# Optimization experiments

Hardware: AMD Instinct MI355X
Metric: run time of the kernel (lower is better)

Reference implementation:

```python
import jax, jax.numpy as jnp
import numpy as np
from functools import partial

T_DEC, T_ENC = 64, 256
B, E, D = 32, 256, 512   # batch, audio_encoder_size(=input_size), decoder_hidden_size
N_MEL = 80               # spectral_size == n_mel_channels


def setup_inputs() -> dict:
    key = jax.random.key(0)
    ks = jax.random.split(key, 9)
    s = 0.02
    return {
        "decoder_inputs": jax.random.normal(ks[0], (T_DEC, B, E), jnp.float32),
        "alignment_inputs": jax.random.normal(ks[1], (T_ENC, B, E), jnp.float32),
        "W_att": jax.random.normal(ks[2], (E, D), jnp.float32) * s,      # LinearNorm(D->E, no bias)
        "W_ih": jax.random.normal(ks[3], (3 * D, 2 * E), jnp.float32) * s,  # GRUCell input weights (r,z,n)
        "W_hh": jax.random.normal(ks[4], (3 * D, D), jnp.float32) * s,      # GRUCell hidden weights
        "W_mel": jax.random.normal(ks[5], (N_MEL, D + E), jnp.float32) * s,
        "b_mel": jax.random.normal(ks[6], (N_MEL,), jnp.float32) * s,
        "W_gate": jax.random.normal(ks[7], (1, D + E), jnp.float32) * s,
        "b_gate": jax.random.normal(ks[8], (1,), jnp.float32) * s,
    }


def _decode_loop(decoder_inputs, alignment_inputs, W_att, W_ih, W_hh, W_mel, b_mel, W_gate, b_gate):
    Bd, Dd = decoder_inputs.shape[1], W_hh.shape[1]

    def step(h, dec_in):
        # --- Attention: per-feature softmax over encoder time, collapsed over features ---
        proj = h @ W_att.T                                  # (B, E)
        scores = alignment_inputs * proj[None]              # (T_enc, B, E)
        w = jax.nn.softmax(scores, axis=0)                  # softmax over encoder time
        tw = w.sum(axis=-1)                                 # (T_enc, B): sum of per-feature weights
        ctx = jnp.einsum('tb,tbe->be', tw, alignment_inputs)  # (B, E)
        # --- GRUCell (bias=False) ---
        x = jnp.concatenate([dec_in, ctx], axis=-1)         # (B, 2E)
        gi = x @ W_ih.T                                     # (B, 3D)
        gh = h @ W_hh.T                                     # (B, 3D)
        ir, iz, inn = jnp.split(gi, 3, axis=-1)
        hr, hz, hn = jnp.split(gh, 3, axis=-1)
        r = jax.nn.sigmoid(ir + hr)
        z = jax.nn.sigmoid(iz + hz)
        n = jnp.tanh(inn + r * hn)
        h_new = (1.0 - z) * n + z * h
        h_new = jax.nn.relu(h_new)                          # relu(dropout(h)), dropout=0
        # --- Output heads ---
        dhac = jnp.concatenate([ctx, h_new], axis=-1)       # (B, E+D)
        mel = dhac @ W_mel.T + b_mel                        # (B, N_MEL)
        gate = dhac @ W_gate.T + b_gate                     # (B, 1)
        return h_new, (mel, gate)

    # prepend zero init frame, drop last frame (teacher forcing, T_dec steps)
    init_frame = jnp.zeros((1,) + decoder_inputs.shape[1:], decoder_inputs.dtype)
    seq = jnp.concatenate([init_frame, decoder_inputs[:-1]], axis=0)
    h0 = jnp.zeros((Bd, Dd), decoder_inputs.dtype)
    _, (mels, gates) = jax.lax.scan(step, h0, seq)
    # parse_decoder_outputs
    n_mel = W_mel.shape[0]
    mel_out = mels.transpose(1, 0, 2).reshape(Bd, -1, n_mel).transpose(0, 2, 1)  # (B, n_mel, T_dec)
    gate_out = gates.transpose(1, 0, 2)                                          # (B, T_dec, 1)
    return mel_out, gate_out


def reference(decoder_inputs, alignment_inputs, W_att, W_ih, W_hh, W_mel, b_mel, W_gate, b_gate):
    return _decode_loop(decoder_inputs, alignment_inputs, W_att, W_ih, W_hh,
                        W_mel, b_mel, W_gate, b_gate)
```

## Files before the change

### kernel.cpp

```cpp
#include <hip/hip_runtime.h>
#include <hip/hip_bf16.h>


#define LOG2E 1.4426950408889634f
#define FLAGS_MAGIC 0x13572468u
#define SMEM_BYTES 150016
#define NBLK 98

typedef __attribute__((ext_vector_type(8))) short bf8;
typedef __attribute__((ext_vector_type(4))) float f32x4;
typedef __attribute__((ext_vector_type(4))) unsigned u32x4;
typedef unsigned long long ull;

#define EX2(x) exp2f(x)
#define MFMA16(a, b, c) __builtin_amdgcn_mfma_f32_16x16x32_bf16(a, b, c, 0, 0, 0)

struct Params {
  const float* dec;
  const float* ali;
  const float* watt;
  const float* wih;
  const float* whh;
  const float* wmel;
  const float* bmel;
  const float* wgate;
  const float* bgate;
  float* out;
  unsigned* bar;
  __hip_bfloat16* wihb;
  __hip_bfloat16* whhb;
  __hip_bfloat16* wmelgb;
  __hip_bfloat16* seqb;
  __hip_bfloat16* hbf;
  __hip_bfloat16* ctxb;
  unsigned* wattp;
};

__device__ __forceinline__ bf8 ldfrag(const __hip_bfloat16* p) { return *(const bf8*)p; }
__device__ __forceinline__ float sigm(float x) { return 1.0f / (1.0f + EX2(-x * LOG2E)); }
__device__ __forceinline__ float tanhfast(float x) {
  x = fminf(fmaxf(x, -15.0f), 15.0f);
  float e = EX2(x * (2.0f * LOG2E));
  return (e - 1.0f) / (e + 1.0f);
}
__device__ __forceinline__ float btof(unsigned v) { return __uint_as_float(v << 16); }
__device__ __forceinline__ unsigned short f2bfbits(float x) {
  __hip_bfloat16 h = __float2bfloat16(x);
  return *(unsigned short*)&h;
}
__device__ __forceinline__ unsigned sysld32(const unsigned* p) {
  return __hip_atomic_load(p, __ATOMIC_RELAXED, __HIP_MEMORY_SCOPE_SYSTEM);
}
__device__ __forceinline__ ull sysld64(const ull* p) {
  return __hip_atomic_load(p, __ATOMIC_RELAXED, __HIP_MEMORY_SCOPE_SYSTEM);
}
__device__ __forceinline__ void sysst32(unsigned* p, unsigned v) {
  __hip_atomic_store(p, v, __ATOMIC_RELAXED, __HIP_MEMORY_SCOPE_SYSTEM);
}
__device__ __forceinline__ void sysst64(ull* p, ull v) {
  __hip_atomic_store(p, v, __ATOMIC_RELAXED, __HIP_MEMORY_SCOPE_SYSTEM);
}
__device__ __forceinline__ void sysld16x4(u32x4* d0, u32x4* d1, u32x4* d2, u32x4* d3,
                                          const void* p0, const void* p1,
                                          const void* p2, const void* p3) {
  u32x4 a, b, c, d;
  asm volatile(
      "global_load_dwordx4 %0, %4, off sc0 sc1\n\t"
      "global_load_dwordx4 %1, %5, off sc0 sc1\n\t"
      "global_load_dwordx4 %2, %6, off sc0 sc1\n\t"
      "global_load_dwordx4 %3, %7, off sc0 sc1\n\t"
      "s_waitcnt vmcnt(0)"
      : "=&v"(a), "=&v"(b), "=&v"(c), "=&v"(d)
      : "v"(p0), "v"(p1), "v"(p2), "v"(p3)
      : "memory");
  *d0 = a; *d1 = b; *d2 = c; *d3 = d;
}
__device__ __forceinline__ void waitge(unsigned* w, unsigned tgt) {
  while (sysld32(w) < tgt) __builtin_amdgcn_s_sleep(1);
}

__device__ __forceinline__ void p0bar(unsigned* bar) {
  __syncthreads();
  if (threadIdx.x == 0) {
    __builtin_amdgcn_fence(__ATOMIC_RELEASE, "agent");
    __hip_atomic_fetch_add(bar + 16, 1u, __ATOMIC_RELAXED, __HIP_MEMORY_SCOPE_SYSTEM);
    while (sysld32(bar + 16) < (unsigned)NBLK) __builtin_amdgcn_s_sleep(1);
    __builtin_amdgcn_fence(__ATOMIC_ACQUIRE, "agent");
  }
  __syncthreads();
}

__device__ __forceinline__ void p0a_worker(const Params& p, int wid) {
  for (int i = wid; i < 2252800; i += 17408) {
    if (i < 786432) {
      p.wihb[i] = __float2bfloat16(p.wih[i]);
    } else if (i < 1572864) {
      int j = i - 786432;
      p.whhb[j] = __float2bfloat16(p.whh[j]);
    } else if (i < 2097152) {
      int j = i - 1572864;
      int s = j >> 13;
      p.seqb[j] = (s == 0) ? __float2bfloat16(0.0f) : __float2bfloat16(p.dec[j - 8192]);
    } else if (i < 2170880) {
      int j = i - 2097152;
      int r = j / 768, c = j - r * 768;
      float v = (r < 80) ? p.wmel[j] : ((r == 80) ? p.wgate[c] : 0.0f);
      p.wmelgb[j] = __float2bfloat16(v);
    } else if (i < 2236416) {
      int j = i - 2170880;
      int kp = j >> 8, e = j & 255;
      unsigned lo = f2bfbits(p.watt[e * 512 + 2 * kp]);
      unsigned hi = f2bfbits(p.watt[e * 512 + 2 * kp + 1]);
      p.wattp[j] = lo | (hi << 16);
    } else {
      int j = i - 2236416;
      p.hbf[j] = __float2bfloat16(0.0f);
    }
  }
}

__device__ __forceinline__ void stage_h_frag(__hip_bfloat16* hA,
                                             const __hip_bfloat16* hsrc, int tid) {
  const int lm = tid & 15, lq = (tid >> 4) & 3, wq = tid >> 6;
  const int dst_in = (lq * 16 + lm) * 8;
  const int i0 = wq, i1 = 8 + wq, i2 = 16 + wq, i3 = 24 + wq;
  auto soff = [&](int idx) {
    return ((idx >> 4) * 16 + lm) * 512 + (idx & 15) * 32 + lq * 8;
  };
  u32x4 a, b, c, d;
  sysld16x4(&a, &b, &c, &d, hsrc + soff(i0), hsrc + soff(i1), hsrc + soff(i2),
            hsrc + soff(i3));
  u32x4* dst = (u32x4*)hA;
  dst[(i0 * 512 + dst_in) >> 3] = a;
  dst[(i1 * 512 + dst_in) >> 3] = b;
  dst[(i2 * 512 + dst_in) >> 3] = c;
  dst[(i3 * 512 + dst_in) >> 3] = d;
}
__device__ __forceinline__ void stage_c2(__hip_bfloat16* cA,
                                         const __hip_bfloat16* csrc, int tid) {
  const int lm = tid & 15, lq = (tid >> 4) & 3, wq = tid >> 6;
  const int dst_in = (lq * 16 + lm) * 8;
  const int i0 = wq, i1 = 8 + wq, i2 = 16 + wq, i3 = 24 + wq;
  auto soff = [&](int idx) {
    int bb = (idx >> 4) * 16 + lm;
    int k = (idx & 15) * 32 + lq * 8;
    return ((k >> 8) * 32 + bb) * 256 + (k & 255);
  };
  u32x4 a, b, c, d;
  sysld16x4(&a, &b, &c, &d, csrc + soff(i0), csrc + soff(i1), csrc + soff(i2),
            csrc + soff(i3));
  u32x4* dst = (u32x4*)cA;
  dst[(i0 * 512 + dst_in) >> 3] = a;
  dst[(i1 * 512 + dst_in) >> 3] = b;
  dst[(i2 * 512 + dst_in) >> 3] = c;
  dst[(i3 * 512 + dst_in) >> 3] = d;
}

__global__ void __launch_bounds__(512, 1) rdec_kernel(Params p) {
  const int tid = threadIdx.x;
  const int bid = blockIdx.x;
  extern __shared__ char smem[];
  unsigned* hdone = p.bar + 32;
  unsigned* ctxdone = p.bar + 544;
  unsigned* meldone = p.bar + 1568;

  if (bid == 0) {
    for (int i = 1 + tid; i < 2624; i += 512) sysst32(p.bar + i, 0u);
    __syncthreads();
    if (tid == 0) sysst32(p.bar, FLAGS_MAGIC);
  }

  if (bid < 64) {
    const int b = bid >> 1, eh = bid & 1, hb = eh * 32 + b;
    unsigned short* alds = (unsigned short*)smem;
    float* fb = (float*)(smem + 133120);
    float* shh = fb;
    float* p2 = fb + 512;
    float* rz = fb + 640;
    float* red = fb + 768;
    float* twp = fb + 1280;
    float* tw = fb + 3328;
    float* cp = fb + 3584;
    unsigned short* pc16 = (unsigned short*)(fb + 4096);

    const int el = tid & 127, q = tid >> 7;
    const int eg = tid >> 6, tg = tid & 63;
    const int f = tid & 255, th = tid >> 8;

    for (int i = tid; i < 65536; i += 512) {
      int t = i >> 8, ee = i & 255;
      alds[ee * 260 + t] = f2bfbits(p.ali[t * 8192 + b * 256 + ee]);
    }
    if (tid == 0) {
      while (sysld32(p.bar) != FLAGS_MAGIC) __builtin_amdgcn_s_sleep(1);
    }
    p0bar(p.bar);
    unsigned wr[64];
#pragma unroll
    for (int i = 0; i < 64; ++i) wr[i] = p.wattp[(q * 64 + i) * 256 + eh * 128 + el];

    for (int s = 0; s < 64; ++s) {
      if (tid < 32) waitge(hdone + tid * 16, (unsigned)s);
      else if (tid < 34) waitge(meldone + (tid - 32) * 16, (s >= 4) ? (unsigned)(s - 3) : 0u);
      __syncthreads();
      if (tid < 128) {
        ull w = sysld64((const ull*)(p.hbf + (s & 3) * 16384 + b * 512) + tid);
        shh[tid * 4 + 0] = btof((unsigned)(w & 0xffff));
        shh[tid * 4 + 1] = btof((unsigned)((w >> 16) & 0xffff));
        shh[tid * 4 + 2] = btof((unsigned)((w >> 32) & 0xffff));
        shh[tid * 4 + 3] = btof((unsigned)((w >> 48) & 0xffff));
      }
      __syncthreads();
      {
        const float2* h2 = (const float2*)shh;
        float a0 = 0.f, a1 = 0.f;
#pragma unroll
        for (int i = 0; i < 64; i += 2) {
          unsigned w0 = wr[i], w1 = wr[i + 1];
          float2 h0 = h2[q * 64 + i], h1 = h2[q * 64 + i + 1];
          a0 = fmaf(__uint_as_float(w0 << 16), h0.x, a0);
          a0 = fmaf(__uint_as_float(w0 & 0xffff0000u), h0.y, a0);
          a1 = fmaf(__uint_as_float(w1 << 16), h1.x, a1);
          a1 = fmaf(__uint_as_float(w1 & 0xffff0000u), h1.y, a1);
        }
        red[q * 128 + el] = a0 + a1;
      }
      __syncthreads();
      if (tid < 128)
        p2[tid] = (red[tid] + red[128 + tid] + red[256 + tid] + red[384 + tid]) * LOG2E;
      __syncthreads();
      {
        const unsigned short* ap = alds + (eh * 128 + el) * 260 + q * 64;
        const float pp = p2[el];
        float z0 = 0.f, z1 = 0.f;
#pragma unroll 4
        for (int j = 0; j < 16; ++j) {
          ushort4 v = *(const ushort4*)(ap + j * 4);
          z0 += EX2(btof(v.x) * pp) + EX2(btof(v.y) * pp);
          z1 += EX2(btof(v.z) * pp) + EX2(btof(v.w) * pp);
        }
        red[q * 128 + el] = z0 + z1;
      }
      __syncthreads();
      if (tid < 128)
        rz[tid] = 1.0f / (red[tid] + red[128 + tid] + red[256 + tid] + red[384 + tid]);
      __syncthreads();
      {
        float t0 = 0.f, t1 = 0.f, t2 = 0.f, t3 = 0.f;
#pragma unroll 4
        for (int j = 0; j < 16; ++j) {
          const int e2 = eg * 16 + j;
          ushort4 v = *(const ushort4*)(alds + (eh * 128 + e2) * 260 + tg * 4);
          const float pp = p2[e2], rr = rz[e2];
          t0 = fmaf(EX2(btof(v.x) * pp), rr, t0);
          t1 = fmaf(EX2(btof(v.y) * pp), rr, t1);
          t2 = fmaf(EX2(btof(v.z) * pp), rr, t2);
          t3 = fmaf(EX2(btof(v.w) * pp), rr, t3);
        }
        *(float4*)(twp + eg * 256 + tg * 4) = make_float4(t0, t1, t2, t3);
      }
      __syncthreads();
      if (tid < 256) {
        float t0 = 0.f;
#pragma unroll
        for (int g = 0; g < 8; ++g) t0 += twp[g * 256 + tid];
        tw[tid] = t0;
      }
      __syncthreads();
      {
        const unsigned short* ap = alds + f * 260 + th * 128;
        const float4* twv = (const float4*)(tw + th * 128);
        float c0 = 0.f, c1 = 0.f;
#pragma unroll 4
        for (int j = 0; j < 32; ++j) {
          ushort4 v = *(const ushort4*)(ap + j * 4);
          float4 t4 = twv[j];
          c0 += t4.x * btof(v.x) + t4.y * btof(v.y);
          c1 += t4.z * btof(v.z) + t4.w * btof(v.w);
        }
        cp[th * 256 + f] = c0 + c1;
      }
      __syncthreads();
      if (tid < 256) pc16[tid] = f2bfbits(cp[tid] + cp[256 + tid]);
      __syncthreads();
      if (tid < 32) {
        ull* cs = (ull*)(p.ctxb + ((s & 3) * 64 + hb) * 256);
        const ull* ca = (const ull*)pc16;
        sysst64(cs + tid * 2, ca[tid * 2]);
        sysst64(cs + tid * 2 + 1, ca[tid * 2 + 1]);
      }
      __syncthreads();
      if (tid == 0) sysst32(ctxdone + hb * 16, (unsigned)(s + 1));
    }
  } else if (bid < 96) {
    const int dt = bid - 64;
    const int wv = tid >> 6;
    const bool act = wv < 6;
    const int l = tid & 63, lm = l & 15, lq = l >> 4;
    const int g = wv % 3, mt = wv / 3;
    const int am = mt * 16 + lm;
    const int brow = g * 512 + dt * 16 + lm;
    __hip_bfloat16* hA = (__hip_bfloat16*)smem;
    __hip_bfloat16* cA = (__hip_bfloat16*)(smem + 32768);
    float* pw = (float*)(smem + 65536);
    unsigned short* h16 = (unsigned short*)(smem + 74240);
    p0a_worker(p, (bid - 64) * 512 + tid);
    if (tid == 0) {
      while (sysld32(p.bar) != FLAGS_MAGIC) __builtin_amdgcn_s_sleep(1);
    }
    p0bar(p.bar);
    bf8 WH[16], WD[8], WC[8];
    if (act) {
#pragma unroll
      for (int kt = 0; kt < 16; ++kt) WH[kt] = ldfrag(p.whhb + brow * 512 + kt * 32 + lq * 8);
#pragma unroll
      for (int kt = 0; kt < 8; ++kt) WD[kt] = ldfrag(p.wihb + brow * 512 + kt * 32 + lq * 8);
#pragma unroll
      for (int kt = 0; kt < 8; ++kt) WC[kt] = ldfrag(p.wihb + brow * 512 + 256 + kt * 32 + lq * 8);
    }
    for (int s = 0; s < 64; ++s) {
      if (tid < 32) waitge(hdone + tid * 16, (unsigned)s);
      else if (tid < 34) waitge(meldone + (tid - 32) * 16, (s >= 4) ? (unsigned)(s - 3) : 0u);
      __syncthreads();
      stage_h_frag(hA, p.hbf + (s & 3) * 16384, tid);
      __syncthreads();
      f32x4 acc = {0.f, 0.f, 0.f, 0.f};
      f32x4 gi = {0.f, 0.f, 0.f, 0.f};
      if (act) {
#pragma unroll
        for (int kt = 0; kt < 16; ++kt) {
          bf8 a = ldfrag(hA + (mt * 16 + kt) * 512 + l * 8);
          acc = MFMA16(a, WH[kt], acc);
        }
        const __hip_bfloat16* seqp = p.seqb + s * 8192;
#pragma unroll
        for (int kt = 0; kt < 8; ++kt) {
          bf8 a = ldfrag(seqp + am * 256 + kt * 32 + lq * 8);
          gi = MFMA16(a, WD[kt], gi);
        }
      }
      if (tid < 64) waitge(ctxdone + tid * 16, (unsigned)(s + 1));
      __syncthreads();
      stage_c2(cA, p.ctxb + (s & 3) * 16384, tid);
      __syncthreads();
      if (act) {
#pragma unroll
        for (int kt = 0; kt < 16; ++kt) {
          bf8 a = ldfrag(cA + (mt * 16 + kt) * 512 + l * 8);
          gi = MFMA16(a, WC[kt & 7], gi);
        }
        if (g < 2) {
#pragma unroll
          for (int r = 0; r < 4; ++r) pw[(wv * 16 + lq * 4 + r) * 17 + lm] = acc[r] + gi[r];
        } else {
#pragma unroll
          for (int r = 0; r < 4; ++r) pw[(wv * 16 + lq * 4 + r) * 17 + lm] = acc[r];
#pragma unroll
          for (int r = 0; r < 4; ++r) pw[((6 + mt) * 16 + lq * 4 + r) * 17 + lm] = gi[r];
        }
      }
      __syncthreads();
      {
        const int bb = tid >> 4, dl = tid & 15;
        const int mtb = bb >> 4, bl = bb & 15;
        float rg = sigm(pw[((mtb * 3 + 0) * 16 + bl) * 17 + dl]);
        float zg = sigm(pw[((mtb * 3 + 1) * 16 + bl) * 17 + dl]);
        float hn = pw[((mtb * 3 + 2) * 16 + bl) * 17 + dl];
        float inn = pw[((6 + mtb) * 16 + bl) * 17 + dl];
        float nn = tanhfast(fmaf(rg, hn, inn));
        const int d = dt * 16 + dl;
        float ho = btof(((unsigned short*)hA)[((bb >> 4) * 16 + (d >> 5)) * 512 +
                                              (((d >> 3) & 3) * 16 + (bb & 15)) * 8 +
                                              (d & 7)]);
        float hnew = fmaxf(0.0f, fmaf(zg, ho - nn, nn));
        h16[bb * 16 + dl] = f2bfbits(hnew);
      }
      __syncthreads();
      if (tid < 256) {
        const int bb2 = tid >> 3, dp = tid & 7;
        unsigned v = (unsigned)h16[bb2 * 16 + dp * 2] |
                     ((unsigned)h16[bb2 * 16 + dp * 2 + 1] << 16);
        sysst32((unsigned*)(p.hbf + ((s + 1) & 3) * 16384) + bb2 * 256 + dt * 8 + dp, v);
      }
      __syncthreads();
      if (tid == 0) sysst32(hdone + dt * 16, (unsigned)(s + 1));
    }
  } else {
    const int mt = bid - 96;
    const int wv = tid >> 6;
    const bool act = wv < 6;
    const int l = tid & 63, lm = l & 15, lq = l >> 4;
    const int nt = wv;
    const int bn = nt * 16 + lm;
    __hip_bfloat16* hA = (__hip_bfloat16*)smem;
    __hip_bfloat16* cA = (__hip_bfloat16*)(smem + 32768);
    p0a_worker(p, (bid - 64) * 512 + tid);
    if (tid == 0) {
      while (sysld32(p.bar) != FLAGS_MAGIC) __builtin_amdgcn_s_sleep(1);
    }
    p0bar(p.bar);
    bf8 WMC[8], WMH[16];
    float bias = 0.f;
    if (act) {
#pragma unroll
      for (int kt = 0; kt < 8; ++kt) WMC[kt] = ldfrag(p.wmelgb + bn * 768 + kt * 32 + lq * 8);
#pragma unroll
      for (int kt = 0; kt < 16; ++kt)
        WMH[kt] = ldfrag(p.wmelgb + bn * 768 + 256 + kt * 32 + lq * 8);
      bias = (bn < 80) ? p.bmel[bn] : ((bn == 80) ? p.bgate[0] : 0.f);
    }
    for (int tau = 0; tau < 64; ++tau) {
      if (tid < 32) waitge(hdone + tid * 16, (unsigned)(tau + 1));
      else if (tid >= 64 && tid < 128) waitge(ctxdone + (tid - 64) * 16, (unsigned)(tau + 1));
      __syncthreads();
      stage_h_frag(hA, p.hbf + ((tau + 1) & 3) * 16384, tid);
      stage_c2(cA, p.ctxb + (tau & 3) * 16384, tid);
      __syncthreads();
      if (act) {
        f32x4 acc = {0.f, 0.f, 0.f, 0.f};
#pragma unroll
        for (int kt = 0; kt < 32; ++kt) {
          bf8 a = (kt < 16) ? ldfrag(cA + (mt * 16 + kt) * 512 + l * 8)
                            : ldfrag(hA + (mt * 16 + (kt - 16)) * 512 + l * 8);
          bf8 bb2 = (kt < 16) ? WMC[kt & 7] : WMH[kt - 16];
          acc = MFMA16(a, bb2, acc);
        }
#pragma unroll
        for (int r = 0; r < 4; ++r) {
          int bb = mt * 16 + lq * 4 + r;
          float v = acc[r] + bias;
          if (bn < 80)
            p.out[bb * 5120 + bn * 64 + tau] = v;
          else if (bn == 80)
            p.out[163840 + bb * 64 + tau] = v;
        }
      }
      __syncthreads();
      if (tid == 0) sysst32(meldone + mt * 16, (unsigned)(tau + 1));
    }
  }
}

extern "C" void kernel_launch(void* const* d_in, const int* in_sizes, int n_in,
                              void* d_out, int out_size, void* d_ws, size_t ws_size,
                              hipStream_t stream) {
  Params P;
  P.dec = (const float*)d_in[0];
  P.ali = (const float*)d_in[1];
  P.watt = (const float*)d_in[2];
  P.wih = (const float*)d_in[3];
  P.whh = (const float*)d_in[4];
  P.wmel = (const float*)d_in[5];
  P.bmel = (const float*)d_in[6];
  P.wgate = (const float*)d_in[7];
  P.bgate = (const float*)d_in[8];
  P.out = (float*)d_out;

  char* w = (char*)d_ws;
  size_t o = 0;
  auto nxt = [&](size_t b) {
    char* r = w + o;
    o += (b + 255) & ~(size_t)255;
    return r;
  };
  P.bar = (unsigned*)nxt(16384);
  P.wihb = (__hip_bfloat16*)nxt(1536 * 512 * 2);
  P.whhb = (__hip_bfloat16*)nxt(1536 * 512 * 2);
  P.wmelgb = (__hip_bfloat16*)nxt(96 * 768 * 2);
  P.seqb = (__hip_bfloat16*)nxt(64 * 32 * 256 * 2);
  P.hbf = (__hip_bfloat16*)nxt(4 * 32 * 512 * 2);
  P.ctxb = (__hip_bfloat16*)nxt(4 * 64 * 256 * 2);
  P.wattp = (unsigned*)nxt(256 * 256 * 4);

  (void)hipFuncSetAttribute((const void*)rdec_kernel,
                            hipFuncAttributeMaxDynamicSharedMemorySize, SMEM_BYTES);

  void* args[] = {&P};
  hipError_t err = hipLaunchCooperativeKernel((void*)rdec_kernel, dim3(NBLK), dim3(512),
                                              args, SMEM_BYTES, stream);
  if (err != hipSuccess) {
    rdec_kernel<<<dim3(NBLK), dim3(512), SMEM_BYTES, stream>>>(P);
  }
}
```

Baseline: 925.6 us.

## Split attention across four blocks per batch and use shuffle reductions

The attention stage now runs on 128 blocks instead of 64, with each block covering a quarter of the feature dimension rather than half. This shortens the serial per-step critical path. Within a block, the LDS reductions and their extra barriers are replaced by 8-lane shuffle-xor reductions. The cost is more partial context vectors to publish, wait on and sum via MFMA in the GRU and mel blocks, plus more flags to poll. The grid grows to 162 cooperative blocks, which must all be co-resident on the device.

```diff
diff --git a/kernel.cpp b/kernel.cpp
--- a/kernel.cpp
+++ b/kernel.cpp
@@ -4,8 +4,8 @@
 
 #define LOG2E 1.4426950408889634f
 #define FLAGS_MAGIC 0x13572468u
-#define SMEM_BYTES 150016
-#define NBLK 98
+#define SMEM_BYTES 138752
+#define NBLK 162
 
 typedef __attribute__((ext_vector_type(8))) short bf8;
 typedef __attribute__((ext_vector_type(4))) float f32x4;
@@ -136,24 +136,29 @@
   dst[(i2 * 512 + dst_in) >> 3] = c;
   dst[(i3 * 512 + dst_in) >> 3] = d;
 }
-__device__ __forceinline__ void stage_c2(__hip_bfloat16* cA,
+__device__ __forceinline__ void stage_c4(__hip_bfloat16* cA,
                                          const __hip_bfloat16* csrc, int tid) {
   const int lm = tid & 15, lq = (tid >> 4) & 3, wq = tid >> 6;
   const int dst_in = (lq * 16 + lm) * 8;
-  const int i0 = wq, i1 = 8 + wq, i2 = 16 + wq, i3 = 24 + wq;
+  u32x4* dst = (u32x4*)cA;
   auto soff = [&](int idx) {
-    int bb = (idx >> 4) * 16 + lm;
-    int k = (idx & 15) * 32 + lq * 8;
+    int mt = idx >> 5, kt = idx & 31;
+    int bb = mt * 16 + lm;
+    int k = kt * 32 + lq * 8;
     return ((k >> 8) * 32 + bb) * 256 + (k & 255);
   };
-  u32x4 a, b, c, d;
-  sysld16x4(&a, &b, &c, &d, csrc + soff(i0), csrc + soff(i1), csrc + soff(i2),
-            csrc + soff(i3));
-  u32x4* dst = (u32x4*)cA;
-  dst[(i0 * 512 + dst_in) >> 3] = a;
-  dst[(i1 * 512 + dst_in) >> 3] = b;
-  dst[(i2 * 512 + dst_in) >> 3] = c;
-  dst[(i3 * 512 + dst_in) >> 3] = d;
+#pragma unroll
+  for (int r = 0; r < 2; ++r) {
+    const int i0 = (4 * r + 0) * 8 + wq, i1 = (4 * r + 1) * 8 + wq;
+    const int i2 = (4 * r + 2) * 8 + wq, i3 = (4 * r + 3) * 8 + wq;
+    u32x4 a, b, c, d;
+    sysld16x4(&a, &b, &c, &d, csrc + soff(i0), csrc + soff(i1), csrc + soff(i2),
+              csrc + soff(i3));
+    dst[(i0 * 512 + dst_in) >> 3] = a;
+    dst[(i1 * 512 + dst_in) >> 3] = b;
+    dst[(i2 * 512 + dst_in) >> 3] = c;
+    dst[(i3 * 512 + dst_in) >> 3] = d;
+  }
 }
 
 __global__ void __launch_bounds__(512, 1) rdec_kernel(Params p) {
@@ -162,7 +167,7 @@
   extern __shared__ char smem[];
   unsigned* hdone = p.bar + 32;
   unsigned* ctxdone = p.bar + 544;
-  unsigned* meldone = p.bar + 1568;
+  unsigned* meldone = p.bar + 2592;
 
   if (bid == 0) {
     for (int i = 1 + tid; i < 2624; i += 512) sysst32(p.bar + i, 0u);
@@ -170,21 +175,17 @@
     if (tid == 0) sysst32(p.bar, FLAGS_MAGIC);
   }
 
-  if (bid < 64) {
-    const int b = bid >> 1, eh = bid & 1, hb = eh * 32 + b;
+  if (bid < 128) {
+    const int b = bid >> 2, q4 = bid & 3, hb = q4 * 32 + b;
     unsigned short* alds = (unsigned short*)smem;
     float* fb = (float*)(smem + 133120);
     float* shh = fb;
-    float* p2 = fb + 512;
-    float* rz = fb + 640;
-    float* red = fb + 768;
-    float* twp = fb + 1280;
-    float* tw = fb + 3328;
-    float* cp = fb + 3584;
-    unsigned short* pc16 = (unsigned short*)(fb + 4096);
-
-    const int el = tid & 127, q = tid >> 7;
-    const int eg = tid >> 6, tg = tid & 63;
+    float* p2l = fb + 512;
+    float* rzl = fb + 576;
+    float* tw = fb + 640;
+    float* cp = fb + 896;
+
+    const int el = tid >> 3, kq = tid & 7;
     const int f = tid & 255, th = tid >> 8;
 
     for (int i = tid; i < 65536; i += 512) {
@@ -195,9 +196,9 @@
       while (sysld32(p.bar) != FLAGS_MAGIC) __builtin_amdgcn_s_sleep(1);
     }
     p0bar(p.bar);
-    unsigned wr[64];
-#pragma unroll
-    for (int i = 0; i < 64; ++i) wr[i] = p.wattp[(q * 64 + i) * 256 + eh * 128 + el];
+    unsigned wr[32];
+#pragma unroll
+    for (int i = 0; i < 32; ++i) wr[i] = p.wattp[(i * 8 + kq) * 256 + q4 * 64 + el];
 
     for (int s = 0; s < 64; ++s) {
       if (tid < 32) waitge(hdone + tid * 16, (unsigned)s);
@@ -215,56 +216,54 @@
         const float2* h2 = (const float2*)shh;
         float a0 = 0.f, a1 = 0.f;
 #pragma unroll
-        for (int i = 0; i < 64; i += 2) {
+        for (int i = 0; i < 32; i += 2) {
           unsigned w0 = wr[i], w1 = wr[i + 1];
-          float2 h0 = h2[q * 64 + i], h1 = h2[q * 64 + i + 1];
+          float2 h0 = h2[i * 8 + kq], h1 = h2[(i + 1) * 8 + kq];
           a0 = fmaf(__uint_as_float(w0 << 16), h0.x, a0);
           a0 = fmaf(__uint_as_float(w0 & 0xffff0000u), h0.y, a0);
           a1 = fmaf(__uint_as_float(w1 << 16), h1.x, a1);
           a1 = fmaf(__uint_as_float(w1 & 0xffff0000u), h1.y, a1);
         }
-        red[q * 128 + el] = a0 + a1;
-      }
-      __syncthreads();
-      if (tid < 128)
-        p2[tid] = (red[tid] + red[128 + tid] + red[256 + tid] + red[384 + tid]) * LOG2E;
-      __syncthreads();
-      {
-        const unsigned short* ap = alds + (eh * 128 + el) * 260 + q * 64;
-        const float pp = p2[el];
+        float pr = a0 + a1;
+        pr += __shfl_xor(pr, 1);
+        pr += __shfl_xor(pr, 2);
+        pr += __shfl_xor(pr, 4);
+        const float pp = pr * LOG2E;
+        const unsigned short* ap = alds + (q4 * 64 + el) * 260 + kq * 32;
         float z0 = 0.f, z1 = 0.f;
-#pragma unroll 4
-        for (int j = 0; j < 16; ++j) {
+#pragma unroll
+        for (int j = 0; j < 8; ++j) {
           ushort4 v = *(const ushort4*)(ap + j * 4);
           z0 += EX2(btof(v.x) * pp) + EX2(btof(v.y) * pp);
           z1 += EX2(btof(v.z) * pp) + EX2(btof(v.w) * pp);
         }
-        red[q * 128 + el] = z0 + z1;
-      }
-      __syncthreads();
-      if (tid < 128)
-        rz[tid] = 1.0f / (red[tid] + red[128 + tid] + red[256 + tid] + red[384 + tid]);
+        float zz = z0 + z1;
+        zz += __shfl_xor(zz, 1);
+        zz += __shfl_xor(zz, 2);
+        zz += __shfl_xor(zz, 4);
+        if (kq == 0) {
+          p2l[el] = pp;
+          rzl[el] = 1.0f / zz;
+        }
+      }
       __syncthreads();
       {
         float t0 = 0.f, t1 = 0.f, t2 = 0.f, t3 = 0.f;
-#pragma unroll 4
-        for (int j = 0; j < 16; ++j) {
-          const int e2 = eg * 16 + j;
-          ushort4 v = *(const ushort4*)(alds + (eh * 128 + e2) * 260 + tg * 4);
-          const float pp = p2[e2], rr = rz[e2];
-          t0 = fmaf(EX2(btof(v.x) * pp), rr, t0);
-          t1 = fmaf(EX2(btof(v.y) * pp), rr, t1);
-          t2 = fmaf(EX2(btof(v.z) * pp), rr, t2);
-          t3 = fmaf(EX2(btof(v.w) * pp), rr, t3);
-        }
-        *(float4*)(twp + eg * 256 + tg * 4) = make_float4(t0, t1, t2, t3);
-      }
-      __syncthreads();
-      if (tid < 256) {
-        float t0 = 0.f;
-#pragma unroll
-        for (int g = 0; g < 8; ++g) t0 += twp[g * 256 + tid];
-        tw[tid] = t0;
+#pragma unroll
+        for (int j = 0; j < 8; ++j) {
+          const int e2 = kq * 8 + j;
+          ushort4 v = *(const ushort4*)(alds + (q4 * 64 + e2) * 260 + el * 4);
+          const float ppj = p2l[e2], rr = rzl[e2];
+          t0 = fmaf(EX2(btof(v.x) * ppj), rr, t0);
+          t1 = fmaf(EX2(btof(v.y) * ppj), rr, t1);
+          t2 = fmaf(EX2(btof(v.z) * ppj), rr, t2);
+          t3 = fmaf(EX2(btof(v.w) * ppj), rr, t3);
+        }
+        t0 += __shfl_xor(t0, 1); t0 += __shfl_xor(t0, 2); t0 += __shfl_xor(t0, 4);
+        t1 += __shfl_xor(t1, 1); t1 += __shfl_xor(t1, 2); t1 += __shfl_xor(t1, 4);
+        t2 += __shfl_xor(t2, 1); t2 += __shfl_xor(t2, 2); t2 += __shfl_xor(t2, 4);
+        t3 += __shfl_xor(t3, 1); t3 += __shfl_xor(t3, 2); t3 += __shfl_xor(t3, 4);
+        if (kq == 0) *(float4*)(tw + el * 4) = make_float4(t0, t1, t2, t3);
       }
       __syncthreads();
       {
@@ -281,19 +280,18 @@
         cp[th * 256 + f] = c0 + c1;
       }
       __syncthreads();
-      if (tid < 256) pc16[tid] = f2bfbits(cp[tid] + cp[256 + tid]);
-      __syncthreads();
-      if (tid < 32) {
-        ull* cs = (ull*)(p.ctxb + ((s & 3) * 64 + hb) * 256);
-        const ull* ca = (const ull*)pc16;
-        sysst64(cs + tid * 2, ca[tid * 2]);
-        sysst64(cs + tid * 2 + 1, ca[tid * 2 + 1]);
+      if (tid < 128) {
+        float2 ca = ((const float2*)cp)[tid];
+        float2 cb = ((const float2*)(cp + 256))[tid];
+        float cv0 = ca.x + cb.x, cv1 = ca.y + cb.y;
+        unsigned u = (unsigned)f2bfbits(cv0) | ((unsigned)f2bfbits(cv1) << 16);
+        sysst32((unsigned*)(p.ctxb + ((s & 3) * 128 + hb) * 256) + tid, u);
       }
       __syncthreads();
       if (tid == 0) sysst32(ctxdone + hb * 16, (unsigned)(s + 1));
     }
-  } else if (bid < 96) {
-    const int dt = bid - 64;
+  } else if (bid < 160) {
+    const int dt = bid - 128;
     const int wv = tid >> 6;
     const bool act = wv < 6;
     const int l = tid & 63, lm = l & 15, lq = l >> 4;
@@ -302,9 +300,9 @@
     const int brow = g * 512 + dt * 16 + lm;
     __hip_bfloat16* hA = (__hip_bfloat16*)smem;
     __hip_bfloat16* cA = (__hip_bfloat16*)(smem + 32768);
-    float* pw = (float*)(smem + 65536);
-    unsigned short* h16 = (unsigned short*)(smem + 74240);
-    p0a_worker(p, (bid - 64) * 512 + tid);
+    float* pw = (float*)(smem + 98304);
+    unsigned short* h16 = (unsigned short*)(smem + 107008);
+    p0a_worker(p, (bid - 128) * 512 + tid);
     if (tid == 0) {
       while (sysld32(p.bar) != FLAGS_MAGIC) __builtin_amdgcn_s_sleep(1);
     }
@@ -339,14 +337,14 @@
           gi = MFMA16(a, WD[kt], gi);
         }
       }
-      if (tid < 64) waitge(ctxdone + tid * 16, (unsigned)(s + 1));
-      __syncthreads();
-      stage_c2(cA, p.ctxb + (s & 3) * 16384, tid);
+      if (tid < 128) waitge(ctxdone + tid * 16, (unsigned)(s + 1));
+      __syncthreads();
+      stage_c4(cA, p.ctxb + (s & 3) * 32768, tid);
       __syncthreads();
       if (act) {
 #pragma unroll
-        for (int kt = 0; kt < 16; ++kt) {
-          bf8 a = ldfrag(cA + (mt * 16 + kt) * 512 + l * 8);
+        for (int kt = 0; kt < 32; ++kt) {
+          bf8 a = ldfrag(cA + (mt * 32 + kt) * 512 + l * 8);
           gi = MFMA16(a, WC[kt & 7], gi);
         }
         if (g < 2) {
@@ -386,7 +384,7 @@
       if (tid == 0) sysst32(hdone + dt * 16, (unsigned)(s + 1));
     }
   } else {
-    const int mt = bid - 96;
+    const int mt = bid - 160;
     const int wv = tid >> 6;
     const bool act = wv < 6;
     const int l = tid & 63, lm = l & 15, lq = l >> 4;
@@ -394,7 +392,7 @@
     const int bn = nt * 16 + lm;
     __hip_bfloat16* hA = (__hip_bfloat16*)smem;
     __hip_bfloat16* cA = (__hip_bfloat16*)(smem + 32768);
-    p0a_worker(p, (bid - 64) * 512 + tid);
+    p0a_worker(p, (bid - 128) * 512 + tid);
     if (tid == 0) {
       while (sysld32(p.bar) != FLAGS_MAGIC) __builtin_amdgcn_s_sleep(1);
     }
@@ -411,18 +409,18 @@
     }
     for (int tau = 0; tau < 64; ++tau) {
       if (tid < 32) waitge(hdone + tid * 16, (unsigned)(tau + 1));
-      else if (tid >= 64 && tid < 128) waitge(ctxdone + (tid - 64) * 16, (unsigned)(tau + 1));
+      else if (tid >= 64 && tid < 192) waitge(ctxdone + (tid - 64) * 16, (unsigned)(tau + 1));
       __syncthreads();
       stage_h_frag(hA, p.hbf + ((tau + 1) & 3) * 16384, tid);
-      stage_c2(cA, p.ctxb + (tau & 3) * 16384, tid);
+      stage_c4(cA, p.ctxb + (tau & 3) * 32768, tid);
       __syncthreads();
       if (act) {
         f32x4 acc = {0.f, 0.f, 0.f, 0.f};
 #pragma unroll
-        for (int kt = 0; kt < 32; ++kt) {
-          bf8 a = (kt < 16) ? ldfrag(cA + (mt * 16 + kt) * 512 + l * 8)
-                            : ldfrag(hA + (mt * 16 + (kt - 16)) * 512 + l * 8);
-          bf8 bb2 = (kt < 16) ? WMC[kt & 7] : WMH[kt - 16];
+        for (int kt = 0; kt < 48; ++kt) {
+          bf8 a = (kt < 32) ? ldfrag(cA + (mt * 32 + kt) * 512 + l * 8)
+                            : ldfrag(hA + (mt * 16 + (kt - 32)) * 512 + l * 8);
+          bf8 bb2 = (kt < 32) ? WMC[kt & 7] : WMH[kt - 32];
           acc = MFMA16(a, bb2, acc);
         }
 #pragma unroll
@@ -469,7 +467,7 @@
   P.wmelgb = (__hip_bfloat16*)nxt(96 * 768 * 2);
   P.seqb = (__hip_bfloat16*)nxt(64 * 32 * 256 * 2);
   P.hbf = (__hip_bfloat16*)nxt(4 * 32 * 512 * 2);
-  P.ctxb = (__hip_bfloat16*)nxt(4 * 64 * 256 * 2);
+  P.ctxb = (__hip_bfloat16*)nxt(4 * 128 * 256 * 2);
   P.wattp = (unsigned*)nxt(256 * 256 * 4);
 
   (void)hipFuncSetAttribute((const void*)rdec_kernel,
```

Measured after the change: 833.3 us. -10.0%, faster.
